# Performance work log

Hardware: AMD Instinct MI355X
Metric: run time of the kernel (lower is better)

Reference implementation:

```python
import jax, jax.numpy as jnp
import numpy as np

# Dims: E=rows per table, T=num tables, D=embedding dim, B=batch, L=bag size
E, T, D = 200000, 16, 64
B, L = 4096, 20


def setup_inputs() -> dict:
    key = jax.random.key(0)
    k_w, k_i = jax.random.split(key)
    # nn.Parameter(torch.randn(num_embeddings, num_tables, embedding_dim))
    weights = jax.random.normal(k_w, (E, T, D), dtype=jnp.float32)
    sharded_sparse_features = jax.random.randint(k_i, (B, T, L), 0, E, dtype=jnp.int64)
    return {"weights": weights, "sharded_sparse_features": sharded_sparse_features}


def reference(weights, sharded_sparse_features):
    # weights: [E, T, D], indices: [B, T, L] -> out: [B, T, D]
    # Per-table embedding-bag with sum pooling (forward_fast_single).
    w_t = jnp.transpose(weights, (1, 0, 2))  # [T, E, D]

    def per_table(w, idx):  # w: [E, D], idx: [B, L]
        return w[idx].sum(axis=1)  # gather [B, L, D] -> sum over bag -> [B, D]

    return jax.vmap(per_table, in_axes=(0, 1), out_axes=1)(w_t, sharded_sparse_features)
```

## Files before the change

### kernel.cpp

```cpp
#include <hip/hip_runtime.h>


constexpr int E = 200000;
constexpr int T = 16;
constexpr int D = 64;
constexpr int B = 4096;
constexpr int L = 20;

__global__ __launch_bounds__(256) void embed_bag_kernel(
    const float* __restrict__ w,
    const int* __restrict__ idx,
    float* __restrict__ out)
{
    __shared__ int s_idx[T * L];

    const int b   = blockIdx.x;
    const int tid = threadIdx.x;

    const int* __restrict__ slab = idx + (size_t)b * (T * L);
    if (tid < T * L) s_idx[tid] = slab[tid];
    {
        const int k = tid + 256;
        if (k < T * L) s_idx[k] = slab[k];
    }
    __syncthreads();

    const int t   = tid >> 4;
    const int sub = tid & 15;

    const unsigned lane_off = (unsigned)(t * 256 + sub * 16);
    const char* __restrict__ wb = (const char*)w;

    int e[L];
#pragma unroll
    for (int l = 0; l < L; ++l) e[l] = s_idx[t * L + l];

    float4 acc = make_float4(0.f, 0.f, 0.f, 0.f);
#pragma unroll
    for (int l = 0; l < L; ++l) {
        const unsigned off = ((unsigned)e[l] << 12) | lane_off;
        const float4 v = *(const float4*)(wb + off);
        acc.x += v.x; acc.y += v.y; acc.z += v.z; acc.w += v.w;
    }

    *(float4*)(out + ((size_t)(b * T + t) * D) + sub * 4) = acc;
}

extern "C" void kernel_launch(void* const* d_in, const int* in_sizes, int n_in,
                              void* d_out, int out_size, void* d_ws, size_t ws_size,
                              hipStream_t stream) {
    const float* w  = (const float*)d_in[0];
    const int* idx  = (const int*)d_in[1];
    float* out      = (float*)d_out;

    embed_bag_kernel<<<B, 256, 0, stream>>>(w, idx, out);
}
```

Baseline: 923.4 us.

## Split each bag across two half-waves and regroup blocks by table

Reorganises the grid so each block handles one table and eight bags. Each bag's 20 lookups are split between two 16-lane groups that each sum 10 rows, and the halves are combined with a cross-lane shuffle. Indices are read straight from global memory instead of being staged in shared memory, which removes the barrier. Output is written with nontemporal stores. The aim is more memory-level parallelism per thread and possibly better cache locality within a table, at the cost of doubling thread count per bag and adding a shuffle reduction.

After: 928.9 us. Within noise of the previous version (+0.6%).

```diff
diff --git a/kernel.cpp b/kernel.cpp
--- a/kernel.cpp
+++ b/kernel.cpp
@@ -7,43 +7,45 @@
 constexpr int B = 4096;
 constexpr int L = 20;
 
+constexpr int BAGS_PER_BLOCK = 8;
+constexpr int LHALF = L / 2;
+
+typedef float f32x4 __attribute__((ext_vector_type(4)));
+
 __global__ __launch_bounds__(256) void embed_bag_kernel(
     const float* __restrict__ w,
     const int* __restrict__ idx,
     float* __restrict__ out)
 {
-    __shared__ int s_idx[T * L];
+    const int t    = blockIdx.y;
+    const int tid  = threadIdx.x;
+    const int bagl = tid >> 5;
+    const int g    = (tid >> 4) & 1;
+    const int sub  = tid & 15;
+    const int b    = blockIdx.x * BAGS_PER_BLOCK + bagl;
 
-    const int b   = blockIdx.x;
-    const int tid = threadIdx.x;
+    const int* __restrict__ slab = idx + ((size_t)b * T + t) * L + g * LHALF;
 
-    const int* __restrict__ slab = idx + (size_t)b * (T * L);
-    if (tid < T * L) s_idx[tid] = slab[tid];
-    {
-        const int k = tid + 256;
-        if (k < T * L) s_idx[k] = slab[k];
-    }
-    __syncthreads();
-
-    const int t   = tid >> 4;
-    const int sub = tid & 15;
-
-    const unsigned lane_off = (unsigned)(t * 256 + sub * 16);
+    const unsigned lane_off = (unsigned)(t * (D * 4) + sub * 16);
     const char* __restrict__ wb = (const char*)w;
 
-    int e[L];
+    f32x4 acc = {0.f, 0.f, 0.f, 0.f};
 #pragma unroll
-    for (int l = 0; l < L; ++l) e[l] = s_idx[t * L + l];
-
-    float4 acc = make_float4(0.f, 0.f, 0.f, 0.f);
-#pragma unroll
-    for (int l = 0; l < L; ++l) {
-        const unsigned off = ((unsigned)e[l] << 12) | lane_off;
-        const float4 v = *(const float4*)(wb + off);
-        acc.x += v.x; acc.y += v.y; acc.z += v.z; acc.w += v.w;
+    for (int k = 0; k < LHALF; ++k) {
+        const unsigned off = ((unsigned)slab[k] << 12) | lane_off;
+        const f32x4 v = *(const f32x4*)(wb + off);
+        acc += v;
     }
 
-    *(float4*)(out + ((size_t)(b * T + t) * D) + sub * 4) = acc;
+    acc.x += __shfl_xor(acc.x, 16);
+    acc.y += __shfl_xor(acc.y, 16);
+    acc.z += __shfl_xor(acc.z, 16);
+    acc.w += __shfl_xor(acc.w, 16);
+
+    if (g == 0) {
+        f32x4* dst = (f32x4*)(out + ((size_t)b * T + t) * D + sub * 4);
+        __builtin_nontemporal_store(acc, dst);
+    }
 }
 
 extern "C" void kernel_launch(void* const* d_in, const int* in_sizes, int n_in,
@@ -53,5 +55,5 @@
     const int* idx  = (const int*)d_in[1];
     float* out      = (float*)d_out;
 
-    embed_bag_kernel<<<B, 256, 0, stream>>>(w, idx, out);
+    embed_bag_kernel<<<dim3(B / BAGS_PER_BLOCK, T), 256, 0, stream>>>(w, idx, out);
 }
```
